# Kernel optimization log

Measured on AMD Instinct MI355X. Metric: run time of the kernel, lower is better.

The kernel has to match this reference:

```python
import jax, jax.numpy as jnp
import numpy as np

N_GRAPHS = 64

def gcn_conv(x, src, dst, dinv, W, b, num_nodes):
    # PyG GCNConv: transform, then normalized scatter-add aggregation, then bias.
    xw = x @ W                                      # [N, H]
    norm = (dinv[src] * dinv[dst])[:, None]         # [E+N, 1]
    msg = xw[src] * norm                            # gather + scale
    out = jax.ops.segment_sum(msg, dst, num_segments=num_nodes)
    return out + b


def setup_inputs() -> dict:
    key = jax.random.key(0)
    ks = jax.random.split(key, 12)
    N, E, C_in, H, C_out = 100000, 1600000, 128, 128, 64
    x = jax.random.normal(ks[0], (N, C_in), dtype=jnp.float32)
    edge_index = jax.random.randint(ks[1], (2, E), 0, N, dtype=jnp.int64)
    batch = jnp.sort(jax.random.randint(ks[2], (N,), 0, N_GRAPHS, dtype=jnp.int64))
    s = lambda k, shp, fan: jax.random.normal(k, shp, dtype=jnp.float32) / np.sqrt(fan)
    return {
        "x": x, "edge_index": edge_index, "batch": batch,
        "W1": s(ks[3], (C_in, H), C_in), "b1": jnp.zeros((H,), jnp.float32),
        "W2": s(ks[4], (H, H), H),       "b2": jnp.zeros((H,), jnp.float32),
        "Wl1": s(ks[5], (H, C_out), H),  "bl1": jnp.zeros((C_out,), jnp.float32),
        "Wl2": s(ks[6], (C_out, 1), C_out), "bl2": jnp.zeros((1,), jnp.float32),
    }


def reference(x, edge_index, batch, W1, b1, W2, b2, Wl1, bl1, Wl2, bl2):
    N = x.shape[0]
    # add self-loops (GCNConv default)
    loop = jnp.arange(N, dtype=edge_index.dtype)
    src = jnp.concatenate([edge_index[0], loop])
    dst = jnp.concatenate([edge_index[1], loop])
    # symmetric normalization D^{-1/2} A_hat D^{-1/2}
    deg = jax.ops.segment_sum(jnp.ones_like(dst, dtype=x.dtype), dst, num_segments=N)
    dinv = jnp.where(deg > 0, jax.lax.rsqrt(jnp.maximum(deg, 1.0)), 0.0)

    h = jax.nn.relu(gcn_conv(x, src, dst, dinv, W1, b1, N))
    h = gcn_conv(h, src, dst, dinv, W2, b2, N)          # [N, H]

    # global mean pool per graph
    sums = jax.ops.segment_sum(h, batch, num_segments=N_GRAPHS)    # [G, H]
    cnts = jax.ops.segment_sum(jnp.ones((N,), h.dtype), batch, num_segments=N_GRAPHS)
    pooled = sums / jnp.maximum(cnts, 1.0)[:, None]

    out = jax.nn.relu(pooled @ Wl1 + bl1)
    return jax.nn.sigmoid(out @ Wl2 + bl2)              # [G, 1]
```

## Files before the change

### kernel.cpp

```cpp
#include <hip/hip_runtime.h>
#include <hip/hip_bf16.h>
#include <math.h>

typedef unsigned short u16;
typedef unsigned char u8;
typedef unsigned int u32;
typedef unsigned long long u64;
typedef __attribute__((ext_vector_type(8))) short bf16x8;
typedef __attribute__((ext_vector_type(4))) float f32x4;
typedef __attribute__((ext_vector_type(2))) float f32x2;

__device__ __forceinline__ float b2f(u16 u) {
    union { unsigned int i; float f; } v; v.i = ((unsigned int)u) << 16; return v.f;
}
__device__ __forceinline__ u16 f2b(float f) {
    unsigned int i = __float_as_uint(f);
    unsigned int r = (i + 0x7FFFu + ((i >> 16) & 1u)) >> 16;
    return (u16)r;
}
__device__ __forceinline__ f32x2 fp8x2_lo(u32 w) { return __builtin_amdgcn_cvt_pk_f32_fp8((int)w, false); }
__device__ __forceinline__ f32x2 fp8x2_hi(u32 w) { return __builtin_amdgcn_cvt_pk_f32_fp8((int)w, true); }
__device__ __forceinline__ u32 f32x2_to_fp8(float a, float b) {
    return (u32)__builtin_amdgcn_cvt_pk_fp8_f32(a, b, 0, false);
}

#define BSHIFT 9
#define EPB 4096
#define BH_CHUNK 16384
#define SRC_MASK 0x1FFFFu

__global__ __launch_bounds__(256) void k_init(int* __restrict__ bcnt,
                                              int* __restrict__ bkcur,
                                              float* __restrict__ pooled) {
    int t = threadIdx.x;
    int b = blockIdx.x;
    if (b == 0) { bcnt[t] = 0; bkcur[t] = 0; }
    else {
        int i = (b - 1) * 256 + t;
        if (i < 64 * 128) pooled[i] = 0.f;
    }
}

__global__ __launch_bounds__(256) void k_bhist(const int* __restrict__ dst, int E,
                                               int* __restrict__ bcnt, int nbuck) {
    __shared__ int h[256];
    int t = threadIdx.x;
    h[t] = 0;
    __syncthreads();
    int e0 = blockIdx.x * BH_CHUNK;
    int e1 = e0 + BH_CHUNK; if (e1 > E) e1 = E;
    for (int i = e0 + t; i < e1; i += 256) atomicAdd(&h[dst[i] >> BSHIFT], 1);
    __syncthreads();
    if (t < nbuck && h[t] > 0) atomicAdd(&bcnt[t], h[t]);
}

__global__ __launch_bounds__(256) void k_bscan(const int* __restrict__ bcnt,
                                               int* __restrict__ bbase,
                                               int* __restrict__ row_off,
                                               int nbuck, int N, int E) {
    __shared__ int lds[256];
    int t = threadIdx.x;
    int mine = (t < nbuck) ? bcnt[t] : 0;
    lds[t] = mine;
    __syncthreads();
    int val = mine;
    for (int s = 1; s < 256; s <<= 1) {
        int add = (t >= s) ? lds[t - s] : 0;
        __syncthreads();
        val += add;
        lds[t] = val;
        __syncthreads();
    }
    if (t < nbuck) bbase[t] = val - mine;
    if (t == nbuck - 1) bbase[nbuck] = val;
    if (t == 0) row_off[N] = E;
}

__global__ __launch_bounds__(256) void k_bucketA(const int* __restrict__ src,
                                                 const int* __restrict__ dst, int E,
                                                 const int* __restrict__ bbase,
                                                 int* __restrict__ bkcur,
                                                 u32* __restrict__ stage, int nbuck) {
    __shared__ int cntL[512];
    __shared__ int prefE[512];
    __shared__ int allocL[512];
    __shared__ int baseL[512];
    __shared__ u64 stageL[EPB];
    int t = threadIdx.x;
    int e0 = blockIdx.x * EPB;

    for (int i = t; i < 512; i += 256) cntL[i] = 0;
    __syncthreads();
#pragma unroll
    for (int j = 0; j < EPB / 256; j++) {
        int e = e0 + j * 256 + t;
        if (e < E) atomicAdd(&cntL[dst[e] >> BSHIFT], 1);
    }
    __syncthreads();
    for (int i = t; i < 512; i += 256) prefE[i] = cntL[i];
    __syncthreads();
    for (int s = 1; s < 512; s <<= 1) {
        int v0 = (t >= s) ? prefE[t - s] : 0;
        int i1 = t + 256;
        int v1 = (i1 >= s) ? prefE[i1 - s] : 0;
        __syncthreads();
        prefE[t] += v0;
        prefE[i1] += v1;
        __syncthreads();
    }
    for (int i = t; i < 512; i += 256) {
        int ex = prefE[i] - cntL[i];
        prefE[i] = ex;
        allocL[i] = ex;
    }
    __syncthreads();
    for (int i = t; i < 512; i += 256) {
        if (i < nbuck && cntL[i] > 0)
            baseL[i] = bbase[i] + atomicAdd(&bkcur[i], cntL[i]);
    }
    __syncthreads();
#pragma unroll
    for (int j = 0; j < EPB / 256; j++) {
        int e = e0 + j * 256 + t;
        if (e < E) {
            int d = dst[e];
            int b = d >> BSHIFT;
            int slot = atomicAdd(&allocL[b], 1);
            stageL[slot] = ((u64)(unsigned)d << 32) | (unsigned)src[e];
        }
    }
    __syncthreads();
    int tot = E - e0; if (tot > EPB) tot = EPB;
    for (int i = t; i < tot; i += 256) {
        u64 v = stageL[i];
        int b = (int)(v >> (32 + BSHIFT));
        u32 d9 = (u32)((v >> 32) & 511u);
        u32 packed = (d9 << 17) | ((u32)v & SRC_MASK);
        stage[baseL[b] + (i - prefE[b])] = packed;
    }
}

__global__ __launch_bounds__(256) void k_bucketB(const u32* __restrict__ stage,
                                                 const int* __restrict__ bbase,
                                                 int* __restrict__ csr_src,
                                                 int* __restrict__ row_off,
                                                 float* __restrict__ dinv, int N) {
    __shared__ int hist[512];
    __shared__ int pref[512];
    __shared__ int cur[512];
    int b = blockIdx.x, t = threadIdx.x;
    int node_lo = b << BSHIFT;
    int nloc = N - node_lo; if (nloc > 512) nloc = 512;
    int rbeg = bbase[b], rend = bbase[b + 1];

    for (int i = t; i < 512; i += 256) hist[i] = 0;
    __syncthreads();
    for (int i = rbeg + t; i < rend; i += 256) atomicAdd(&hist[stage[i] >> 17], 1);
    __syncthreads();
    for (int i = t; i < 512; i += 256) pref[i] = hist[i];
    __syncthreads();
    for (int s = 1; s < 512; s <<= 1) {
        int v0 = (t >= s) ? pref[t - s] : 0;
        int i1 = t + 256;
        int v1 = (i1 >= s) ? pref[i1 - s] : 0;
        __syncthreads();
        pref[t] += v0;
        pref[i1] += v1;
        __syncthreads();
    }
    for (int i = t; i < 512; i += 256) {
        int ex = pref[i] - hist[i];
        cur[i] = rbeg + ex;
        if (i < nloc) {
            row_off[node_lo + i] = rbeg + ex;
            dinv[node_lo + i] = rsqrtf((float)(hist[i] + 1));
        }
    }
    __syncthreads();
    for (int i = rbeg + t; i < rend; i += 256) {
        u32 v = stage[i];
        int pos = atomicAdd(&cur[v >> 17], 1);
        csr_src[pos] = (int)(v & SRC_MASK);
    }
}

__global__ void k_wt(const float* __restrict__ W1, const float* __restrict__ W2,
                     u16* __restrict__ Wt1, u16* __restrict__ Wt2) {
    const float* W = blockIdx.x ? W2 : W1;
    u16* Wt = blockIdx.x ? Wt2 : Wt1;
    int t = threadIdx.x;
    for (int i = t; i < 16384; i += 256) {
        int k = i >> 7, c = i & 127;
        Wt[c * 128 + k] = f2b(W[i]);
    }
}

template <typename TIN>
__global__ __launch_bounds__(256) void k_gemm_mfma(const TIN* __restrict__ X,
                                                   const u16* __restrict__ Wt,
                                                   const float* __restrict__ dinv,
                                                   u8* __restrict__ Y, int N) {
    __shared__ u16 WtL[128 * 128];
    __shared__ u8 YL[4][16 * 128];
    int t = threadIdx.x;
    {
        const char* gsrc = (const char*)Wt;
        char* lbase = (char*)WtL;
#pragma unroll
        for (int i = 0; i < 8; i++) {
            int byte = (i * 256 + t) * 16;
            int row = byte >> 8;
            int swz = byte ^ ((row & 7) << 4);
            *(uint4*)(lbase + swz) = *(const uint4*)(gsrc + byte);
        }
    }
    __syncthreads();

    int wave = t >> 6, lane = t & 63;
    int lrow = lane & 15, lseg = lane >> 4;
    const char* lbase = (const char*)WtL;
    u8* yw = &YL[wave][0];

#pragma unroll
    for (int rg = 0; rg < 2; rg++) {
        int r0w = blockIdx.x * 128 + rg * 64 + wave * 16;

        bf16x8 a[4];
        {
            int row = r0w + lrow; if (row >= N) row = N - 1;
            if constexpr (sizeof(TIN) == 4) {
                const float* xp = (const float*)X + (size_t)row * 128 + lseg * 8;
#pragma unroll
                for (int j = 0; j < 4; j++) {
                    float4 f0 = *(const float4*)(xp + j * 32);
                    float4 f1 = *(const float4*)(xp + j * 32 + 4);
                    bf16x8 v;
                    v[0] = (short)f2b(f0.x); v[1] = (short)f2b(f0.y);
                    v[2] = (short)f2b(f0.z); v[3] = (short)f2b(f0.w);
                    v[4] = (short)f2b(f1.x); v[5] = (short)f2b(f1.y);
                    v[6] = (short)f2b(f1.z); v[7] = (short)f2b(f1.w);
                    a[j] = v;
                }
            } else {
                const u16* xp = (const u16*)X + (size_t)row * 128 + lseg * 8;
#pragma unroll
                for (int j = 0; j < 4; j++) a[j] = *(const bf16x8*)(xp + j * 32);
            }
        }

        f32x4 acc[8];
#pragma unroll
        for (int c = 0; c < 8; c++) acc[c] = (f32x4){0.f, 0.f, 0.f, 0.f};

#pragma unroll
        for (int c = 0; c < 8; c++) {
            int wrow = c * 16 + lrow;
#pragma unroll
            for (int j = 0; j < 4; j++) {
                int byte = wrow * 256 + (j * 32 + lseg * 8) * 2;
                int swz = byte ^ ((wrow & 7) << 4);
                bf16x8 bf = *(const bf16x8*)(lbase + swz);
                acc[c] = __builtin_amdgcn_mfma_f32_16x16x32_bf16(a[j], bf, acc[c], 0, 0, 0);
            }
        }

        float dv[4];
        int rowb = r0w + lseg * 4;
#pragma unroll
        for (int r = 0; r < 4; r++) {
            int row = rowb + r;
            dv[r] = (row < N) ? dinv[row] : 0.f;
        }
#pragma unroll
        for (int c = 0; c < 8; c++) {
            u32 p01 = f32x2_to_fp8(acc[c][0] * dv[0], acc[c][1] * dv[1]);
            u32 p23 = f32x2_to_fp8(acc[c][2] * dv[2], acc[c][3] * dv[3]);
            int base = (lseg * 4) * 128 + c * 16 + lrow;
            yw[base]           = (u8)p01;
            yw[base + 128]     = (u8)(p01 >> 8);
            yw[base + 256]     = (u8)p23;
            yw[base + 384]     = (u8)(p23 >> 8);
        }
#pragma unroll
        for (int k = 0; k < 2; k++) {
            int idx = lane + 64 * k;
            int row = idx >> 3;
            int seg = idx & 7;
            int grow = r0w + row;
            uint4 v = *(const uint4*)&yw[row * 128 + seg * 16];
            if (grow < N) *(uint4*)&Y[(size_t)grow * 128 + seg * 16] = v;
        }
    }
}

__global__ __launch_bounds__(256) void k_agg(const u8* __restrict__ Z,
                                             const float* __restrict__ dinv,
                                             const int* __restrict__ row_off,
                                             const int* __restrict__ csr_src,
                                             const float* __restrict__ bias,
                                             u16* __restrict__ OUT, int N, int do_relu) {
    int wv = (blockIdx.x * blockDim.x + threadIdx.x) >> 6;
    int lane = threadIdx.x & 63;
    int n0 = wv * 2, n1 = n0 + 1;
    if (n0 >= N) return;
    bool has1 = n1 < N;
    int g = lane >> 4;
    int fb = (lane & 15) * 8;

    int beg0 = row_off[n0], end0 = row_off[n0 + 1];
    int beg1 = beg0, end1 = beg0;
    if (has1) { beg1 = end0; end1 = row_off[n1 + 1]; }

    float acc0[8], acc1[8];
#pragma unroll
    for (int j = 0; j < 8; j++) { acc0[j] = 0.f; acc1[j] = 0.f; }

    if (g == 0) {
        uint2 v = *(const uint2*)&Z[(size_t)n0 * 128 + fb];
        f32x2 f0 = fp8x2_lo(v.x), f1 = fp8x2_hi(v.x);
        f32x2 f2 = fp8x2_lo(v.y), f3 = fp8x2_hi(v.y);
        acc0[0] += f0.x; acc0[1] += f0.y; acc0[2] += f1.x; acc0[3] += f1.y;
        acc0[4] += f2.x; acc0[5] += f2.y; acc0[6] += f3.x; acc0[7] += f3.y;
    }
    if (g == 1 && has1) {
        uint2 v = *(const uint2*)&Z[(size_t)n1 * 128 + fb];
        f32x2 f0 = fp8x2_lo(v.x), f1 = fp8x2_hi(v.x);
        f32x2 f2 = fp8x2_lo(v.y), f3 = fp8x2_hi(v.y);
        acc1[0] += f0.x; acc1[1] += f0.y; acc1[2] += f1.x; acc1[3] += f1.y;
        acc1[4] += f2.x; acc1[5] += f2.y; acc1[6] += f3.x; acc1[7] += f3.y;
    }

    int base0 = beg0, base1 = beg1;
    while (base0 < end0 || base1 < end1) {
        bool h0 = base0 < end0, h1 = base1 < end1;
        int idx0 = 0, idx1 = 0;
        if (h0) { int ii = base0 + lane; if (ii > end0 - 1) ii = end0 - 1; idx0 = csr_src[ii]; }
        if (h1) { int ii = base1 + lane; if (ii > end1 - 1) ii = end1 - 1; idx1 = csr_src[ii]; }
        if (h0) {
            int nc = end0 - base0; if (nc > 64) nc = 64;
#pragma unroll
            for (int k = 0; k < 4; k++) {
                if (k && k * 16 >= nc) break;
                int eo = k * 16 + g;
                int sl = eo < nc ? eo : nc - 1;
                float w = (eo < nc) ? 1.f : 0.f;
                int s = __shfl(idx0, sl, 64);
                uint2 v = *(const uint2*)&Z[(size_t)s * 128 + fb];
                f32x2 f0 = fp8x2_lo(v.x), f1 = fp8x2_hi(v.x);
                f32x2 f2 = fp8x2_lo(v.y), f3 = fp8x2_hi(v.y);
                acc0[0] = fmaf(w, f0.x, acc0[0]); acc0[1] = fmaf(w, f0.y, acc0[1]);
                acc0[2] = fmaf(w, f1.x, acc0[2]); acc0[3] = fmaf(w, f1.y, acc0[3]);
                acc0[4] = fmaf(w, f2.x, acc0[4]); acc0[5] = fmaf(w, f2.y, acc0[5]);
                acc0[6] = fmaf(w, f3.x, acc0[6]); acc0[7] = fmaf(w, f3.y, acc0[7]);
            }
        }
        if (h1) {
            int nc = end1 - base1; if (nc > 64) nc = 64;
#pragma unroll
            for (int k = 0; k < 4; k++) {
                if (k && k * 16 >= nc) break;
                int eo = k * 16 + g;
                int sl = eo < nc ? eo : nc - 1;
                float w = (eo < nc) ? 1.f : 0.f;
                int s = __shfl(idx1, sl, 64);
                uint2 v = *(const uint2*)&Z[(size_t)s * 128 + fb];
                f32x2 f0 = fp8x2_lo(v.x), f1 = fp8x2_hi(v.x);
                f32x2 f2 = fp8x2_lo(v.y), f3 = fp8x2_hi(v.y);
                acc1[0] = fmaf(w, f0.x, acc1[0]); acc1[1] = fmaf(w, f0.y, acc1[1]);
                acc1[2] = fmaf(w, f1.x, acc1[2]); acc1[3] = fmaf(w, f1.y, acc1[3]);
                acc1[4] = fmaf(w, f2.x, acc1[4]); acc1[5] = fmaf(w, f2.y, acc1[5]);
                acc1[6] = fmaf(w, f3.x, acc1[6]); acc1[7] = fmaf(w, f3.y, acc1[7]);
            }
        }
        base0 += 64; base1 += 64;
    }

#pragma unroll
    for (int j = 0; j < 8; j++) {
        acc0[j] += __shfl_xor(acc0[j], 16, 64);
        acc0[j] += __shfl_xor(acc0[j], 32, 64);
        acc1[j] += __shfl_xor(acc1[j], 16, 64);
        acc1[j] += __shfl_xor(acc1[j], 32, 64);
    }

    if (g == 0 || (g == 1 && has1)) {
        int n = (g == 0) ? n0 : n1;
        float din = dinv[n];
        float4 bb0 = *(const float4*)&bias[fb];
        float4 bb1 = *(const float4*)&bias[fb + 4];
        float a[8];
#pragma unroll
        for (int j = 0; j < 8; j++) a[j] = (g == 0) ? acc0[j] : acc1[j];
        float o[8];
        o[0] = din * a[0] + bb0.x; o[1] = din * a[1] + bb0.y;
        o[2] = din * a[2] + bb0.z; o[3] = din * a[3] + bb0.w;
        o[4] = din * a[4] + bb1.x; o[5] = din * a[5] + bb1.y;
        o[6] = din * a[6] + bb1.z; o[7] = din * a[7] + bb1.w;
        if (do_relu) {
#pragma unroll
            for (int j = 0; j < 8; j++) o[j] = fmaxf(o[j], 0.f);
        }
        u16 ob[8];
#pragma unroll
        for (int j = 0; j < 8; j++) ob[j] = f2b(o[j]);
        *(uint4*)&OUT[(size_t)n * 128 + fb] = *(uint4*)ob;
    }
}

__global__ __launch_bounds__(64) void k_pool_partial(const u16* __restrict__ H,
                                                     const int* __restrict__ batch, int N,
                                                     float* __restrict__ pooled) {
    int t = threadIdx.x;
    int chunk = (N + gridDim.x - 1) / gridDim.x;
    int beg = blockIdx.x * chunk;
    int end = beg + chunk; if (end > N) end = N;
    if (beg >= end) return;
    float ax = 0.f, ay = 0.f;
    int g = batch[beg];
    for (int nn = beg; nn < end; ++nn) {
        int gn = batch[nn];
        if (gn != g) {
            atomicAdd(&pooled[g * 128 + 2 * t], ax);
            atomicAdd(&pooled[g * 128 + 2 * t + 1], ay);
            ax = 0.f; ay = 0.f;
            g = gn;
        }
        ushort2 v = *(const ushort2*)&H[(size_t)nn * 128 + 2 * t];
        ax += b2f(v.x); ay += b2f(v.y);
    }
    atomicAdd(&pooled[g * 128 + 2 * t], ax);
    atomicAdd(&pooled[g * 128 + 2 * t + 1], ay);
}

__global__ void k_pool_final(const int* __restrict__ batch, int N,
                             float* __restrict__ pooled) {
    int g = blockIdx.x;
    int t = threadIdx.x;
    __shared__ int sh[2];
    if (t == 0) {
        int lo = 0, hi = N;
        while (lo < hi) { int m = (lo + hi) >> 1; if (batch[m] < g) lo = m + 1; else hi = m; }
        sh[0] = lo;
        lo = 0; hi = N;
        while (lo < hi) { int m = (lo + hi) >> 1; if (batch[m] < g + 1) lo = m + 1; else hi = m; }
        sh[1] = lo;
    }
    __syncthreads();
    float cnt = (float)(sh[1] - sh[0]);
    if (cnt < 1.f) cnt = 1.f;
    pooled[g * 128 + t] /= cnt;
}

__global__ void k_mlp(const float* __restrict__ pooled, const float* __restrict__ Wl1,
                      const float* __restrict__ bl1, const float* __restrict__ Wl2,
                      const float* __restrict__ bl2, float* __restrict__ out) {
    int g = blockIdx.x;
    int j = threadIdx.x;
    float acc = 0.f;
#pragma unroll 8
    for (int k = 0; k < 128; k++) acc += pooled[g * 128 + k] * Wl1[k * 64 + j];
    float h = fmaxf(acc + bl1[j], 0.f);
    float v = h * Wl2[j];
#pragma unroll
    for (int off = 32; off > 0; off >>= 1) v += __shfl_down(v, off);
    if (j == 0) out[g] = 1.f / (1.f + expf(-(v + bl2[0])));
}

extern "C" void kernel_launch(void* const* d_in, const int* in_sizes, int n_in,
                              void* d_out, int out_size, void* d_ws, size_t ws_size,
                              hipStream_t stream) {
    const float* x    = (const float*)d_in[0];
    const int*   edge = (const int*)d_in[1];
    const int*   batch= (const int*)d_in[2];
    const float* W1   = (const float*)d_in[3];
    const float* b1   = (const float*)d_in[4];
    const float* W2   = (const float*)d_in[5];
    const float* b2   = (const float*)d_in[6];
    const float* Wl1  = (const float*)d_in[7];
    const float* bl1  = (const float*)d_in[8];
    const float* Wl2  = (const float*)d_in[9];
    const float* bl2  = (const float*)d_in[10];
    float* out = (float*)d_out;

    int N = in_sizes[0] / 128;
    int E = in_sizes[1] / 2;
    const int* src = edge;
    const int* dst = edge + E;
    int nbuck = (N + (1 << BSHIFT) - 1) >> BSHIFT;

    char* ws = (char*)d_ws;
    size_t off = 0;
    auto alloc = [&](size_t bytes) { void* p = ws + off; off += (bytes + 511) & ~(size_t)511; return p; };
    float* dinv    = (float*)alloc((size_t)N * 4);
    u8*    Z       = (u8*)alloc((size_t)N * 128);
    u16*   H       = (u16*)alloc((size_t)N * 128 * 2);
    int*   row_off = (int*)alloc((size_t)(N + 1) * 4);
    int*   csr_src = (int*)alloc((size_t)E * 4);
    u32*   stage   = (u32*)alloc((size_t)E * 4);
    int*   bcnt    = (int*)alloc(256 * 4);
    int*   bbase   = (int*)alloc(260 * 4);
    int*   bkcur   = (int*)alloc(256 * 4);
    float* pooled  = (float*)alloc(64 * 128 * 4);
    u16*   Wt1     = (u16*)alloc(128 * 128 * 2);
    u16*   Wt2     = (u16*)alloc(128 * 128 * 2);

    k_init<<<1 + (64 * 128 + 255) / 256, 256, 0, stream>>>(bcnt, bkcur, pooled);
    k_bhist<<<(E + BH_CHUNK - 1) / BH_CHUNK, 256, 0, stream>>>(dst, E, bcnt, nbuck);
    k_bscan<<<1, 256, 0, stream>>>(bcnt, bbase, row_off, nbuck, N, E);
    k_wt<<<2, 256, 0, stream>>>(W1, W2, Wt1, Wt2);
    k_bucketA<<<(E + EPB - 1) / EPB, 256, 0, stream>>>(src, dst, E, bbase, bkcur, stage, nbuck);
    k_bucketB<<<nbuck, 256, 0, stream>>>(stage, bbase, csr_src, row_off, dinv, N);

    k_gemm_mfma<float><<<(N + 127) / 128, 256, 0, stream>>>(x, Wt1, dinv, Z, N);
    k_agg<<<(N + 7) / 8, 256, 0, stream>>>(Z, dinv, row_off, csr_src, b1, H, N, 1);
    k_gemm_mfma<u16><<<(N + 127) / 128, 256, 0, stream>>>(H, Wt2, dinv, Z, N);
    k_agg<<<(N + 7) / 8, 256, 0, stream>>>(Z, dinv, row_off, csr_src, b2, H, N, 0);
    k_pool_partial<<<2048, 64, 0, stream>>>(H, batch, N, pooled);
    k_pool_final<<<64, 128, 0, stream>>>(batch, N, pooled);
    k_mlp<<<64, 64, 0, stream>>>(pooled, Wl1, bl1, Wl2, bl2, out);
}
```

Baseline: 212.5 us.

## Interleave two-node gathers in aggregation and widen CSR bucket kernels to 512 threads

The aggregation inner loop now handles the edge chunks of both destination nodes in one combined loop. It issues both nodes' gathers in each iteration, with step-4 edge offsets, so more independent loads are in flight and the separate per-node branches go away. The bucket-sort kernels move to 512-thread blocks, so each thread owns one of the 512 bucket slots. That makes the scans single-element with fewer loop passes. The risks are masked duplicate loads when the two nodes have very different degrees, and higher per-block resource use.

```diff
diff --git a/kernel.cpp b/kernel.cpp
--- a/kernel.cpp
+++ b/kernel.cpp
@@ -76,7 +76,7 @@
     if (t == 0) row_off[N] = E;
 }
 
-__global__ __launch_bounds__(256) void k_bucketA(const int* __restrict__ src,
+__global__ __launch_bounds__(512) void k_bucketA(const int* __restrict__ src,
                                                  const int* __restrict__ dst, int E,
                                                  const int* __restrict__ bbase,
                                                  int* __restrict__ bkcur,
@@ -89,39 +89,34 @@
     int t = threadIdx.x;
     int e0 = blockIdx.x * EPB;
 
-    for (int i = t; i < 512; i += 256) cntL[i] = 0;
-    __syncthreads();
-#pragma unroll
-    for (int j = 0; j < EPB / 256; j++) {
-        int e = e0 + j * 256 + t;
+    cntL[t] = 0;
+    __syncthreads();
+#pragma unroll
+    for (int j = 0; j < EPB / 512; j++) {
+        int e = e0 + j * 512 + t;
         if (e < E) atomicAdd(&cntL[dst[e] >> BSHIFT], 1);
     }
     __syncthreads();
-    for (int i = t; i < 512; i += 256) prefE[i] = cntL[i];
-    __syncthreads();
+    int mine = cntL[t];
+    prefE[t] = mine;
+    __syncthreads();
+    int val = mine;
     for (int s = 1; s < 512; s <<= 1) {
-        int v0 = (t >= s) ? prefE[t - s] : 0;
-        int i1 = t + 256;
-        int v1 = (i1 >= s) ? prefE[i1 - s] : 0;
+        int add = (t >= s) ? prefE[t - s] : 0;
         __syncthreads();
-        prefE[t] += v0;
-        prefE[i1] += v1;
+        val += add;
+        prefE[t] = val;
         __syncthreads();
     }
-    for (int i = t; i < 512; i += 256) {
-        int ex = prefE[i] - cntL[i];
-        prefE[i] = ex;
-        allocL[i] = ex;
-    }
-    __syncthreads();
-    for (int i = t; i < 512; i += 256) {
-        if (i < nbuck && cntL[i] > 0)
-            baseL[i] = bbase[i] + atomicAdd(&bkcur[i], cntL[i]);
-    }
-    __syncthreads();
-#pragma unroll
-    for (int j = 0; j < EPB / 256; j++) {
-        int e = e0 + j * 256 + t;
+    int ex = val - mine;
+    prefE[t] = ex;
+    allocL[t] = ex;
+    if (t < nbuck && mine > 0)
+        baseL[t] = bbase[t] + atomicAdd(&bkcur[t], mine);
+    __syncthreads();
+#pragma unroll
+    for (int j = 0; j < EPB / 512; j++) {
+        int e = e0 + j * 512 + t;
         if (e < E) {
             int d = dst[e];
             int b = d >> BSHIFT;
@@ -131,7 +126,7 @@
     }
     __syncthreads();
     int tot = E - e0; if (tot > EPB) tot = EPB;
-    for (int i = t; i < tot; i += 256) {
+    for (int i = t; i < tot; i += 512) {
         u64 v = stageL[i];
         int b = (int)(v >> (32 + BSHIFT));
         u32 d9 = (u32)((v >> 32) & 511u);
@@ -140,7 +135,7 @@
     }
 }
 
-__global__ __launch_bounds__(256) void k_bucketB(const u32* __restrict__ stage,
+__global__ __launch_bounds__(512) void k_bucketB(const u32* __restrict__ stage,
                                                  const int* __restrict__ bbase,
                                                  int* __restrict__ csr_src,
                                                  int* __restrict__ row_off,
@@ -153,31 +148,29 @@
     int nloc = N - node_lo; if (nloc > 512) nloc = 512;
     int rbeg = bbase[b], rend = bbase[b + 1];
 
-    for (int i = t; i < 512; i += 256) hist[i] = 0;
-    __syncthreads();
-    for (int i = rbeg + t; i < rend; i += 256) atomicAdd(&hist[stage[i] >> 17], 1);
-    __syncthreads();
-    for (int i = t; i < 512; i += 256) pref[i] = hist[i];
-    __syncthreads();
+    hist[t] = 0;
+    __syncthreads();
+    for (int i = rbeg + t; i < rend; i += 512) atomicAdd(&hist[stage[i] >> 17], 1);
+    __syncthreads();
+    int mine = hist[t];
+    pref[t] = mine;
+    __syncthreads();
+    int val = mine;
     for (int s = 1; s < 512; s <<= 1) {
-        int v0 = (t >= s) ? pref[t - s] : 0;
-        int i1 = t + 256;
-        int v1 = (i1 >= s) ? pref[i1 - s] : 0;
+        int add = (t >= s) ? pref[t - s] : 0;
         __syncthreads();
-        pref[t] += v0;
-        pref[i1] += v1;
+        val += add;
+        pref[t] = val;
         __syncthreads();
     }
-    for (int i = t; i < 512; i += 256) {
-        int ex = pref[i] - hist[i];
-        cur[i] = rbeg + ex;
-        if (i < nloc) {
-            row_off[node_lo + i] = rbeg + ex;
-            dinv[node_lo + i] = rsqrtf((float)(hist[i] + 1));
-        }
-    }
-    __syncthreads();
-    for (int i = rbeg + t; i < rend; i += 256) {
+    int ex = val - mine;
+    cur[t] = rbeg + ex;
+    if (t < nloc) {
+        row_off[node_lo + t] = rbeg + ex;
+        dinv[node_lo + t] = rsqrtf((float)(mine + 1));
+    }
+    __syncthreads();
+    for (int i = rbeg + t; i < rend; i += 512) {
         u32 v = stage[i];
         int pos = atomicAdd(&cur[v >> 17], 1);
         csr_src[pos] = (int)(v & SRC_MASK);
@@ -332,18 +325,26 @@
 
     int base0 = beg0, base1 = beg1;
     while (base0 < end0 || base1 < end1) {
-        bool h0 = base0 < end0, h1 = base1 < end1;
+        int nc0 = 0, nc1 = 0;
         int idx0 = 0, idx1 = 0;
-        if (h0) { int ii = base0 + lane; if (ii > end0 - 1) ii = end0 - 1; idx0 = csr_src[ii]; }
-        if (h1) { int ii = base1 + lane; if (ii > end1 - 1) ii = end1 - 1; idx1 = csr_src[ii]; }
-        if (h0) {
-            int nc = end0 - base0; if (nc > 64) nc = 64;
-#pragma unroll
-            for (int k = 0; k < 4; k++) {
-                if (k && k * 16 >= nc) break;
-                int eo = k * 16 + g;
-                int sl = eo < nc ? eo : nc - 1;
-                float w = (eo < nc) ? 1.f : 0.f;
+        if (base0 < end0) {
+            nc0 = end0 - base0; if (nc0 > 64) nc0 = 64;
+            int ii = base0 + lane; if (ii > end0 - 1) ii = end0 - 1;
+            idx0 = csr_src[ii];
+        }
+        if (base1 < end1) {
+            nc1 = end1 - base1; if (nc1 > 64) nc1 = 64;
+            int ii = base1 + lane; if (ii > end1 - 1) ii = end1 - 1;
+            idx1 = csr_src[ii];
+        }
+        int ncm = nc0 > nc1 ? nc0 : nc1;
+#pragma unroll 4
+        for (int k = 0; k < 16; k++) {
+            if ((k << 2) >= ncm) break;
+            int eo = (k << 2) + g;
+            {
+                int sl = eo < nc0 ? eo : (nc0 > 0 ? nc0 - 1 : 0);
+                float w = (eo < nc0) ? 1.f : 0.f;
                 int s = __shfl(idx0, sl, 64);
                 uint2 v = *(const uint2*)&Z[(size_t)s * 128 + fb];
                 f32x2 f0 = fp8x2_lo(v.x), f1 = fp8x2_hi(v.x);
@@ -353,15 +354,9 @@
                 acc0[4] = fmaf(w, f2.x, acc0[4]); acc0[5] = fmaf(w, f2.y, acc0[5]);
                 acc0[6] = fmaf(w, f3.x, acc0[6]); acc0[7] = fmaf(w, f3.y, acc0[7]);
             }
-        }
-        if (h1) {
-            int nc = end1 - base1; if (nc > 64) nc = 64;
-#pragma unroll
-            for (int k = 0; k < 4; k++) {
-                if (k && k * 16 >= nc) break;
-                int eo = k * 16 + g;
-                int sl = eo < nc ? eo : nc - 1;
-                float w = (eo < nc) ? 1.f : 0.f;
+            {
+                int sl = eo < nc1 ? eo : (nc1 > 0 ? nc1 - 1 : 0);
+                float w = (eo < nc1) ? 1.f : 0.f;
                 int s = __shfl(idx1, sl, 64);
                 uint2 v = *(const uint2*)&Z[(size_t)s * 128 + fb];
                 f32x2 f0 = fp8x2_lo(v.x), f1 = fp8x2_hi(v.x);
@@ -508,8 +503,8 @@
     k_bhist<<<(E + BH_CHUNK - 1) / BH_CHUNK, 256, 0, stream>>>(dst, E, bcnt, nbuck);
     k_bscan<<<1, 256, 0, stream>>>(bcnt, bbase, row_off, nbuck, N, E);
     k_wt<<<2, 256, 0, stream>>>(W1, W2, Wt1, Wt2);
-    k_bucketA<<<(E + EPB - 1) / EPB, 256, 0, stream>>>(src, dst, E, bbase, bkcur, stage, nbuck);
-    k_bucketB<<<nbuck, 256, 0, stream>>>(stage, bbase, csr_src, row_off, dinv, N);
+    k_bucketA<<<(E + EPB - 1) / EPB, 512, 0, stream>>>(src, dst, E, bbase, bkcur, stage, nbuck);
+    k_bucketB<<<nbuck, 512, 0, stream>>>(stage, bbase, csr_src, row_off, dinv, N);
 
     k_gemm_mfma<float><<<(N + 127) / 128, 256, 0, stream>>>(x, Wt1, dinv, Z, N);
     k_agg<<<(N + 7) / 8, 256, 0, stream>>>(Z, dinv, row_off, csr_src, b1, H, N, 1);
```

After: 222.4 us. 1.05x slower.
